# Kernel tuning notes

Hardware: AMD Instinct MI355X
Metric: run time of the kernel (lower is better)

Reference implementation:

```python
import jax, jax.numpy as jnp
import numpy as np

B, N, E, F, G = 32, 512, 4, 128, 64
EMB, HID = 128, 256  # NodeEmbedding: Linear(E*G=256 -> 256) + BN + ELU + Linear(256 -> 128)
NUM_EDGES = 8192
BN_EPS = 1e-5


def setup_inputs() -> dict:
    key = jax.random.key(0)
    ks = jax.random.split(key, 8)
    X = jax.random.normal(ks[0], (B, N, F), dtype=jnp.float32)
    edges = jax.random.randint(ks[1], (B, E, 2, NUM_EDGES), 0, N, dtype=jnp.int64)
    # per-edge-type projection W_e: [F, G] (glorot)
    Ws = jax.random.normal(ks[2], (E, F, G), dtype=jnp.float32) * np.sqrt(2.0 / (F + G))
    # attention vectors a_e: [2G, 1]
    a = jax.random.normal(ks[3], (E, 2 * G, 1), dtype=jnp.float32) * (1.414 * np.sqrt(2.0 / (2 * G + 1)))
    lin0_w = jax.random.normal(ks[4], (E * G, HID), dtype=jnp.float32) * np.sqrt(2.0 / (E * G + HID))
    lin0_b = jnp.zeros((HID,), dtype=jnp.float32)
    bn_gamma = jnp.ones((HID,), dtype=jnp.float32)
    bn_beta = jnp.zeros((HID,), dtype=jnp.float32)
    lin1_w = jax.random.normal(ks[5], (HID, EMB), dtype=jnp.float32) * np.sqrt(2.0 / (HID + EMB))
    lin1_b = jnp.zeros((EMB,), dtype=jnp.float32)
    return {"X": X, "edges": edges, "Ws": Ws, "a": a, "lin0_w": lin0_w,
            "lin0_b": lin0_b, "bn_gamma": bn_gamma, "bn_beta": bn_beta,
            "lin1_w": lin1_w, "lin1_b": lin1_b}


def _dense_adj(edges):
    # COO -> dense, summing duplicates like torch.sparse_coo_tensor(...).to_dense()
    b_ix = jnp.arange(B)[:, None, None]
    e_ix = jnp.arange(E)[None, :, None]
    src = edges[:, :, 0, :]
    dst = edges[:, :, 1, :]
    A = jnp.zeros((B, E, N, N), dtype=jnp.float32)
    return A.at[b_ix, e_ix, src, dst].add(1.0)


def reference(X, edges, Ws, a, lin0_w, lin0_b, bn_gamma, bn_beta, lin1_w, lin1_b):
    A = _dense_adj(edges)                                   # [B,E,N,N]
    Wh = jnp.einsum('bnf,efg->beng', X, Ws)                 # [B,E,N,G]
    Wh1 = jnp.einsum('beng,ego->beno', Wh, a[:, :G, :])     # [B,E,N,1]
    Wh2 = jnp.einsum('beng,ego->beno', Wh, a[:, G:, :])     # [B,E,N,1]
    scores = (Wh1 + jnp.swapaxes(Wh2, 2, 3)) * A            # [B,E,N,N] (masked-to-0, NOT -inf: faithful)
    att = jax.nn.softmax(scores, axis=-1)
    H = jnp.einsum('benm,bemg->beng', att * A, Wh)          # [B,E,N,G]
    H = jnp.transpose(H, (0, 2, 1, 3)).reshape(B * N, E * G)
    # NodeEmbedding MLP (BatchNorm1d in training mode: batch stats, biased var)
    h = H @ lin0_w + lin0_b
    mu = jnp.mean(h, axis=0)
    var = jnp.mean((h - mu) ** 2, axis=0)
    h = (h - mu) * jax.lax.rsqrt(var + BN_EPS) * bn_gamma + bn_beta
    h = jax.nn.elu(h)
    out = h @ lin1_w + lin1_b
    return out.reshape(B, N, EMB)
```

## Files before the change

### kernel.cpp

```cpp
#include <hip/hip_runtime.h>

#define Bx 32
#define Nx 512
#define Ex 4
#define Fx 128
#define Gx 64
#define HIDx 256
#define EMBx 128
#define NEDGE 8192

typedef __attribute__((ext_vector_type(8))) short bf16x8;
typedef __attribute__((ext_vector_type(4))) float f32x4;

__device__ __forceinline__ ushort f2bf(float x) {
    unsigned int u = __float_as_uint(x);
    u += 0x7fffu + ((u >> 16) & 1u);
    return (ushort)(u >> 16);
}
__device__ __forceinline__ float bf2f(ushort h) {
    return __uint_as_float(((unsigned int)h) << 16);
}

__global__ __launch_bounds__(256) void k0_convert(const float* __restrict__ w0,
                                                  const float* __restrict__ w1,
                                                  ushort* __restrict__ W0T,
                                                  ushort* __restrict__ W1T) {
    int j = blockIdx.x, k = threadIdx.x;
    if (j < HIDx) {
        W0T[j * HIDx + k] = f2bf(w0[k * HIDx + j]);
    } else {
        int jj = j - HIDx;
        W1T[jj * HIDx + k] = f2bf(w1[k * EMBx + jj]);
    }
}

__global__ __launch_bounds__(256) void k1_wh(const float* __restrict__ X,
                                             const float* __restrict__ Ws,
                                             const float* __restrict__ a,
                                             ushort* __restrict__ Whb,
                                             float* __restrict__ w1,
                                             float* __restrict__ w2) {
    __shared__ float sXT[Fx][68];
    __shared__ float red1[16][68];
    __shared__ float red2[16][68];
    int id = blockIdx.x;
    int e = id & 3;
    int rest = id >> 2;
    int tile = rest & 7;
    int b = rest >> 3;
    int be = b * 4 + e;
    int n0 = tile * 64;
    int tid = threadIdx.x;
    for (int i = tid; i < 64 * Fx; i += 256) {
        int n = i >> 7, k = i & 127;
        sXT[k][n] = X[(size_t)(b * Nx + n0 + n) * Fx + k];
    }
    __syncthreads();
    const float* We = Ws + e * Fx * Gx;
    int gq = tid & 15, nq = tid >> 4;
    int gg = gq * 4, nn = nq * 4;
    float acc[4][4];
    #pragma unroll
    for (int i = 0; i < 4; ++i)
        #pragma unroll
        for (int j = 0; j < 4; ++j) acc[i][j] = 0.f;
    #pragma unroll 4
    for (int k = 0; k < Fx; ++k) {
        float4 av = *(const float4*)&sXT[k][nn];
        float4 bv = *(const float4*)&We[k * Gx + gg];
        float ai[4] = {av.x, av.y, av.z, av.w};
        float bj[4] = {bv.x, bv.y, bv.z, bv.w};
        #pragma unroll
        for (int i = 0; i < 4; ++i)
            #pragma unroll
            for (int j = 0; j < 4; ++j) acc[i][j] += ai[i] * bj[j];
    }
    float a1[4], a2[4];
    #pragma unroll
    for (int j = 0; j < 4; ++j) {
        a1[j] = a[e * 2 * Gx + gg + j];
        a2[j] = a[e * 2 * Gx + Gx + gg + j];
    }
    #pragma unroll
    for (int j = 0; j < 4; ++j) {
        ushort4 v;
        v.x = f2bf(acc[0][j]); v.y = f2bf(acc[1][j]);
        v.z = f2bf(acc[2][j]); v.w = f2bf(acc[3][j]);
        *(ushort4*)&Whb[((size_t)be * Gx + gg + j) * Nx + n0 + nn] = v;
    }
    #pragma unroll
    for (int i = 0; i < 4; ++i) {
        float p1 = acc[i][0] * a1[0] + acc[i][1] * a1[1] + acc[i][2] * a1[2] + acc[i][3] * a1[3];
        float p2 = acc[i][0] * a2[0] + acc[i][1] * a2[1] + acc[i][2] * a2[2] + acc[i][3] * a2[3];
        red1[gq][nn + i] = p1;
        red2[gq][nn + i] = p2;
    }
    __syncthreads();
    if (tid < 64) {
        float s1 = 0.f, s2 = 0.f;
        #pragma unroll
        for (int t = 0; t < 16; ++t) { s1 += red1[t][tid]; s2 += red2[t][tid]; }
        w1[be * Nx + tid + n0] = s1;
        w2[be * Nx + tid + n0] = s2;
    }
}

__global__ __launch_bounds__(512) void k2_att(const int* __restrict__ edges,
                                              const ushort* __restrict__ Whb,
                                              const float* __restrict__ w1g,
                                              const float* __restrict__ w2g,
                                              ushort* __restrict__ Hb) {
    __shared__ ushort P[32 * 512];
    __shared__ float sw2s[512];
    __shared__ float sw1[32];
    __shared__ float sinv[32];
    unsigned int* cnt = (unsigned int*)P;
    int be = blockIdx.x; int b = be >> 2; int e = be & 3;
    int n0 = blockIdx.y * 32;
    int tid = threadIdx.x;
    for (int i = tid; i < 32 * 132; i += 512) cnt[i] = 0u;
    sw2s[tid ^ (((tid >> 5) & 7) << 2)] = w2g[be * Nx + tid];
    if (tid < 32) sw1[tid] = w1g[be * Nx + n0 + tid];
    __syncthreads();
    const int4* srcp = (const int4*)(edges + (size_t)be * 2 * NEDGE);
    const int4* dstp = (const int4*)(edges + (size_t)be * 2 * NEDGE + NEDGE);
    for (int i = tid; i < NEDGE / 4; i += 512) {
        int4 s4 = srcp[i]; int4 d4 = dstp[i];
        int ss[4] = {s4.x, s4.y, s4.z, s4.w};
        int dd[4] = {d4.x, d4.y, d4.z, d4.w};
        #pragma unroll
        for (int u = 0; u < 4; ++u) {
            unsigned int r = (unsigned int)(ss[u] - n0);
            if (r < 32u) atomicAdd(&cnt[r * 132 + (dd[u] >> 2)], 1u << ((dd[u] & 3) * 8));
        }
    }
    __syncthreads();
    int r = tid >> 4, c = tid & 15;
    unsigned int w0_[8];
    const unsigned int* crow = cnt + r * 132 + c * 8;
    #pragma unroll
    for (int i = 0; i < 8; ++i) w0_[i] = crow[i];
    float w1v = sw1[r];
    float mx = 0.f; int K = 0;
    #pragma unroll
    for (int t = 0; t < 8; ++t) {
        unsigned int cw = w0_[t];
        int m0 = c * 32 + t * 4;
        float4 s2 = *(const float4*)&sw2s[m0 ^ ((c & 7) << 2)];
        float ssv[4] = {s2.x, s2.y, s2.z, s2.w};
        #pragma unroll
        for (int jj = 0; jj < 4; ++jj) {
            int cc = (cw >> (jj * 8)) & 255;
            if (cc) { mx = fmaxf(mx, (w1v + ssv[jj]) * (float)cc); K++; }
        }
    }
    #pragma unroll
    for (int off = 1; off < 16; off <<= 1) {
        mx = fmaxf(mx, __shfl_xor(mx, off, 64));
        K += __shfl_xor(K, off, 64);
    }
    __syncthreads();
    float dsum = 0.f;
    #pragma unroll
    for (int tp = 0; tp < 4; ++tp) {
        unsigned int pkw[4];
        #pragma unroll
        for (int h = 0; h < 2; ++h) {
            unsigned int cw = (h == 0) ? w0_[tp * 2] : w0_[tp * 2 + 1];
            int m0 = c * 32 + (tp * 2 + h) * 4;
            float4 s2 = *(const float4*)&sw2s[m0 ^ ((c & 7) << 2)];
            float ssv[4] = {s2.x, s2.y, s2.z, s2.w};
            unsigned int lo = 0, hi = 0;
            #pragma unroll
            for (int jj = 0; jj < 4; ++jj) {
                int cc = (cw >> (jj * 8)) & 255;
                float s = (w1v + ssv[jj]) * (float)cc;
                float ew = __expf(s - mx);
                ew = cc ? ew : 0.f;
                dsum += ew;
                unsigned int pb = cc ? (unsigned int)f2bf(ew * (float)cc) : 0u;
                if (jj & 2) hi |= pb << ((jj & 1) * 16);
                else        lo |= pb << ((jj & 1) * 16);
            }
            pkw[h * 2] = lo; pkw[h * 2 + 1] = hi;
        }
        uint4 pk = {pkw[0], pkw[1], pkw[2], pkw[3]};
        unsigned int byteo = ((unsigned int)(r * 1024 + c * 64 + tp * 16)) ^ ((unsigned int)(r & 7) << 4);
        *(uint4*)((char*)P + byteo) = pk;
    }
    #pragma unroll
    for (int off = 1; off < 16; off <<= 1) dsum += __shfl_xor(dsum, off, 64);
    if (c == 0) sinv[r] = 1.f / (dsum + (float)(Nx - K) * __expf(-mx));
    __syncthreads();
    int wave = tid >> 6, lane = tid & 63;
    int wr = wave >> 2, wc = wave & 3;
    int row = wr * 16 + (lane & 15);
    int kgrp = lane >> 4;
    f32x4 acc = {0.f, 0.f, 0.f, 0.f};
    const ushort* WB = Whb + (size_t)be * Gx * Nx;
    int g0 = wc * 16 + (lane & 15);
    const ushort* Bp = WB + (size_t)g0 * Nx + kgrp * 8;
    unsigned int aswz = ((unsigned int)(row & 7)) << 4;
    #pragma unroll
    for (int ks = 0; ks < 16; ++ks) {
        unsigned int abyte = ((unsigned int)(row * 1024 + ks * 64 + kgrp * 16)) ^ aswz;
        bf16x8 af = *(const bf16x8*)((const char*)P + abyte);
        bf16x8 bfv = *(const bf16x8*)(Bp + ks * 32);
        acc = __builtin_amdgcn_mfma_f32_16x16x32_bf16(af, bfv, acc, 0, 0, 0);
    }
    float4 iv = *(const float4*)&sinv[wr * 16 + kgrp * 4];
    float ivv[4] = {iv.x, iv.y, iv.z, iv.w};
    #pragma unroll
    for (int reg = 0; reg < 4; ++reg) {
        int rr = n0 + wr * 16 + kgrp * 4 + reg;
        Hb[((size_t)(b * Nx) + rr) * (Ex * Gx) + e * Gx + wc * 16 + (lane & 15)] =
            f2bf(acc[reg] * ivv[reg]);
    }
}

__global__ __launch_bounds__(256) void k3_lin0(const ushort* __restrict__ Hb,
                                               const ushort* __restrict__ W0T,
                                               const float* __restrict__ lin0_b,
                                               ushort* __restrict__ h_pre,
                                               float* __restrict__ partials) {
    __shared__ float red_s[2][256], red_q[2][256];
    int tid = threadIdx.x, wave = tid >> 6, lane = tid & 63;
    int wr = wave >> 1, wc = wave & 1;
    int row0 = blockIdx.x * 32 + wr * 16;
    int arow = lane & 15, kg = lane >> 4;
    const ushort* A = Hb + (size_t)(row0 + arow) * HIDx;
    f32x4 acc[8];
    #pragma unroll
    for (int t = 0; t < 8; ++t) acc[t] = (f32x4){0.f, 0.f, 0.f, 0.f};
    #pragma unroll
    for (int ks = 0; ks < 8; ++ks) {
        int k0 = ks * 32 + kg * 8;
        bf16x8 af = *(const bf16x8*)&A[k0];
        #pragma unroll
        for (int jt = 0; jt < 8; ++jt) {
            bf16x8 bf = *(const bf16x8*)&W0T[(size_t)(wc * 128 + jt * 16 + arow) * HIDx + k0];
            acc[jt] = __builtin_amdgcn_mfma_f32_16x16x32_bf16(af, bf, acc[jt], 0, 0, 0);
        }
    }
    #pragma unroll
    for (int jt = 0; jt < 8; ++jt) {
        int col = wc * 128 + jt * 16 + arow;
        float b = lin0_b[col];
        float s = 0.f, q = 0.f;
        #pragma unroll
        for (int reg = 0; reg < 4; ++reg) {
            float v = acc[jt][reg] + b;
            h_pre[(size_t)(row0 + kg * 4 + reg) * HIDx + col] = f2bf(v);
            s += v; q += v * v;
        }
        s += __shfl_xor(s, 16, 64); s += __shfl_xor(s, 32, 64);
        q += __shfl_xor(q, 16, 64); q += __shfl_xor(q, 32, 64);
        if (lane < 16) { red_s[wr][col] = s; red_q[wr][col] = q; }
    }
    __syncthreads();
    int j = tid;
    partials[(size_t)blockIdx.x * 2 * HIDx + j] = red_s[0][j] + red_s[1][j];
    partials[(size_t)blockIdx.x * 2 * HIDx + HIDx + j] = red_q[0][j] + red_q[1][j];
}

__global__ __launch_bounds__(256) void k3b_stats(const float* __restrict__ partials,
                                                 const float* __restrict__ gamma,
                                                 const float* __restrict__ beta,
                                                 float* __restrict__ sb) {
    __shared__ float rs[8][32], rq[8][32];
    int jl = threadIdx.x & 31, sl = threadIdx.x >> 5;
    int j = blockIdx.x * 32 + jl;
    float s = 0.f, q = 0.f;
    for (int blk = sl; blk < 512; blk += 8) {
        s += partials[blk * 512 + j];
        q += partials[blk * 512 + 256 + j];
    }
    rs[sl][jl] = s; rq[sl][jl] = q;
    __syncthreads();
    if (threadIdx.x < 32) {
        float S = 0.f, Q = 0.f;
        #pragma unroll
        for (int t = 0; t < 8; ++t) { S += rs[t][jl]; Q += rq[t][jl]; }
        const float invM = 1.f / 16384.f;
        float mu = S * invM;
        float var = fmaxf(Q * invM - mu * mu, 0.f);
        float sc = gamma[j] * rsqrtf(var + 1e-5f);
        sb[j] = sc;
        sb[256 + j] = beta[j] - mu * sc;
    }
}

__global__ __launch_bounds__(256) void k4_lin1(const ushort* __restrict__ h_pre,
                                               const float* __restrict__ sb,
                                               const ushort* __restrict__ W1T,
                                               const float* __restrict__ lin1_b,
                                               float* __restrict__ out) {
    int tid = threadIdx.x, wave = tid >> 6, lane = tid & 63;
    int wr = wave >> 1, wc = wave & 1;
    int row0 = blockIdx.x * 32 + wr * 16;
    int arow = lane & 15, kg = lane >> 4;
    const ushort* A = h_pre + (size_t)(row0 + arow) * HIDx;
    f32x4 acc[4];
    #pragma unroll
    for (int t = 0; t < 4; ++t) acc[t] = (f32x4){0.f, 0.f, 0.f, 0.f};
    #pragma unroll
    for (int ks = 0; ks < 8; ++ks) {
        int k0 = ks * 32 + kg * 8;
        bf16x8 hv = *(const bf16x8*)&A[k0];
        float4 sc0 = *(const float4*)&sb[k0];
        float4 sc1 = *(const float4*)&sb[k0 + 4];
        float4 bi0 = *(const float4*)&sb[256 + k0];
        float4 bi1 = *(const float4*)&sb[256 + k0 + 4];
        float scv[8] = {sc0.x, sc0.y, sc0.z, sc0.w, sc1.x, sc1.y, sc1.z, sc1.w};
        float biv[8] = {bi0.x, bi0.y, bi0.z, bi0.w, bi1.x, bi1.y, bi1.z, bi1.w};
        bf16x8 af;
        #pragma unroll
        for (int u = 0; u < 8; ++u) {
            float v = bf2f((ushort)hv[u]) * scv[u] + biv[u];
            v = v > 0.f ? v : expm1f(v);
            af[u] = (short)f2bf(v);
        }
        #pragma unroll
        for (int jt = 0; jt < 4; ++jt) {
            bf16x8 bf = *(const bf16x8*)&W1T[(size_t)(wc * 64 + jt * 16 + arow) * HIDx + k0];
            acc[jt] = __builtin_amdgcn_mfma_f32_16x16x32_bf16(af, bf, acc[jt], 0, 0, 0);
        }
    }
    #pragma unroll
    for (int jt = 0; jt < 4; ++jt) {
        int col = wc * 64 + jt * 16 + arow;
        float b = lin1_b[col];
        #pragma unroll
        for (int reg = 0; reg < 4; ++reg)
            out[(size_t)(row0 + kg * 4 + reg) * EMBx + col] = acc[jt][reg] + b;
    }
}

extern "C" void kernel_launch(void* const* d_in, const int* in_sizes, int n_in,
                              void* d_out, int out_size, void* d_ws, size_t ws_size,
                              hipStream_t stream) {
    const float* X      = (const float*)d_in[0];
    const int*   edges  = (const int*)d_in[1];
    const float* Ws     = (const float*)d_in[2];
    const float* a      = (const float*)d_in[3];
    const float* lin0_w = (const float*)d_in[4];
    const float* lin0_b = (const float*)d_in[5];
    const float* gamma  = (const float*)d_in[6];
    const float* beta   = (const float*)d_in[7];
    const float* lin1_w = (const float*)d_in[8];
    const float* lin1_b = (const float*)d_in[9];
    float* ws = (float*)d_ws;

    ushort* Whb     = (ushort*)ws;
    ushort* h_pre   = (ushort*)ws;
    ushort* Hb      = (ushort*)(ws + 4194304);
    float*  w1      = ws + 8388608;
    float*  w2      = ws + 8454144;
    ushort* W0T     = (ushort*)(ws + 8388608);
    ushort* W1T     = (ushort*)(ws + 8421376);
    float*  partials= ws + 8519680;
    float*  sb      = ws + 8781824;
    float*  out     = (float*)d_out;

    k1_wh  <<<dim3(1024), 256, 0, stream>>>(X, Ws, a, Whb, w1, w2);
    k2_att <<<dim3(Bx * Ex, Nx / 32), 512, 0, stream>>>(edges, Whb, w1, w2, Hb);
    k0_convert<<<dim3(HIDx + EMBx), 256, 0, stream>>>(lin0_w, lin1_w, W0T, W1T);
    k3_lin0<<<dim3(512), 256, 0, stream>>>(Hb, W0T, lin0_b, h_pre, partials);
    k3b_stats<<<8, 256, 0, stream>>>(partials, gamma, beta, sb);
    k4_lin1<<<dim3(512), 256, 0, stream>>>(h_pre, sb, W1T, lin1_b, out);
}
```

Baseline: 146.9 us.

## Use bf16 MFMA for Wh projection and drop softmax max pass

The Wh = X·W_e projection now runs on bf16 MFMA instructions, using a pre-transposed bf16 copy of Ws produced by the convert kernel, which is moved to run first. The attention-kernel softmax drops the separate max-finding pass: it uses exp2 on log2e-prescaled scores clamped at 120, counts non-zero entries with a byte-wise popcount, and wave priority is raised around the MFMA loop. This cuts fp32 FMA work and one full pass over the count words. In exchange, X and Ws lose precision to bf16, and an unshifted exponent risks overflow or precision loss if scores are large.

```diff
diff --git a/kernel.cpp b/kernel.cpp
--- a/kernel.cpp
+++ b/kernel.cpp
@@ -12,6 +12,8 @@
 typedef __attribute__((ext_vector_type(8))) short bf16x8;
 typedef __attribute__((ext_vector_type(4))) float f32x4;
 
+#define L2E 1.44269504f
+
 __device__ __forceinline__ ushort f2bf(float x) {
     unsigned int u = __float_as_uint(x);
     u += 0x7fffu + ((u >> 16) & 1u);
@@ -22,27 +24,33 @@
 }
 
 __global__ __launch_bounds__(256) void k0_convert(const float* __restrict__ w0,
-                                                  const float* __restrict__ w1,
+                                                  const float* __restrict__ w1f,
+                                                  const float* __restrict__ Wsf,
                                                   ushort* __restrict__ W0T,
-                                                  ushort* __restrict__ W1T) {
+                                                  ushort* __restrict__ W1T,
+                                                  ushort* __restrict__ WsT) {
     int j = blockIdx.x, k = threadIdx.x;
     if (j < HIDx) {
         W0T[j * HIDx + k] = f2bf(w0[k * HIDx + j]);
+    } else if (j < HIDx + EMBx) {
+        int jj = j - HIDx;
+        W1T[jj * HIDx + k] = f2bf(w1f[k * EMBx + jj]);
     } else {
-        int jj = j - HIDx;
-        W1T[jj * HIDx + k] = f2bf(w1[k * EMBx + jj]);
+        int eg = j - (HIDx + EMBx);
+        if (k < Fx) {
+            int e = eg >> 6, g = eg & 63;
+            WsT[eg * Fx + k] = f2bf(Wsf[(e * Fx + k) * Gx + g]);
+        }
     }
 }
 
 __global__ __launch_bounds__(256) void k1_wh(const float* __restrict__ X,
-                                             const float* __restrict__ Ws,
+                                             const ushort* __restrict__ WsT,
                                              const float* __restrict__ a,
                                              ushort* __restrict__ Whb,
                                              float* __restrict__ w1,
                                              float* __restrict__ w2) {
-    __shared__ float sXT[Fx][68];
-    __shared__ float red1[16][68];
-    __shared__ float red2[16][68];
+    __shared__ ushort sXb[64 * 128];
     int id = blockIdx.x;
     int e = id & 3;
     int rest = id >> 2;
@@ -51,57 +59,61 @@
     int be = b * 4 + e;
     int n0 = tile * 64;
     int tid = threadIdx.x;
-    for (int i = tid; i < 64 * Fx; i += 256) {
-        int n = i >> 7, k = i & 127;
-        sXT[k][n] = X[(size_t)(b * Nx + n0 + n) * Fx + k];
-    }
-    __syncthreads();
-    const float* We = Ws + e * Fx * Gx;
-    int gq = tid & 15, nq = tid >> 4;
-    int gg = gq * 4, nn = nq * 4;
-    float acc[4][4];
-    #pragma unroll
-    for (int i = 0; i < 4; ++i)
-        #pragma unroll
-        for (int j = 0; j < 4; ++j) acc[i][j] = 0.f;
-    #pragma unroll 4
-    for (int k = 0; k < Fx; ++k) {
-        float4 av = *(const float4*)&sXT[k][nn];
-        float4 bv = *(const float4*)&We[k * Gx + gg];
-        float ai[4] = {av.x, av.y, av.z, av.w};
-        float bj[4] = {bv.x, bv.y, bv.z, bv.w};
-        #pragma unroll
-        for (int i = 0; i < 4; ++i)
-            #pragma unroll
-            for (int j = 0; j < 4; ++j) acc[i][j] += ai[i] * bj[j];
-    }
-    float a1[4], a2[4];
-    #pragma unroll
-    for (int j = 0; j < 4; ++j) {
-        a1[j] = a[e * 2 * Gx + gg + j];
-        a2[j] = a[e * 2 * Gx + Gx + gg + j];
-    }
-    #pragma unroll
-    for (int j = 0; j < 4; ++j) {
+    for (int i = tid; i < 2048; i += 256) {
+        int row = i >> 5, kq = i & 31;
+        float4 xv = *(const float4*)&X[(size_t)(b * Nx + n0 + row) * Fx + kq * 4];
+        ushort4 hv;
+        hv.x = f2bf(xv.x); hv.y = f2bf(xv.y); hv.z = f2bf(xv.z); hv.w = f2bf(xv.w);
+        unsigned int byteo = ((unsigned int)(row * 256 + kq * 8)) ^ (((unsigned int)(row & 7)) << 4);
+        *(ushort4*)((char*)sXb + byteo) = hv;
+    }
+    __syncthreads();
+    int wave = tid >> 6, lane = tid & 63;
+    int arow = lane & 15, kg = lane >> 4;
+    int row = wave * 16 + arow;
+    f32x4 acc[4];
+    #pragma unroll
+    for (int t = 0; t < 4; ++t) acc[t] = (f32x4){0.f, 0.f, 0.f, 0.f};
+    const ushort* WT = WsT + e * Gx * Fx;
+    unsigned int aswz = ((unsigned int)(row & 7)) << 4;
+    #pragma unroll
+    for (int ks = 0; ks < 4; ++ks) {
+        unsigned int abyte = ((unsigned int)(row * 256 + ks * 64 + kg * 16)) ^ aswz;
+        bf16x8 af = *(const bf16x8*)((const char*)sXb + abyte);
+        #pragma unroll
+        for (int jt = 0; jt < 4; ++jt) {
+            bf16x8 bf = *(const bf16x8*)&WT[(size_t)(jt * 16 + arow) * Fx + ks * 32 + kg * 8];
+            acc[jt] = __builtin_amdgcn_mfma_f32_16x16x32_bf16(af, bf, acc[jt], 0, 0, 0);
+        }
+    }
+    float a1v[4], a2v[4];
+    #pragma unroll
+    for (int jt = 0; jt < 4; ++jt) {
+        a1v[jt] = a[e * 2 * Gx + jt * 16 + arow];
+        a2v[jt] = a[e * 2 * Gx + Gx + jt * 16 + arow];
+    }
+    int m0 = n0 + wave * 16 + kg * 4;
+    #pragma unroll
+    for (int jt = 0; jt < 4; ++jt) {
+        int g = jt * 16 + arow;
         ushort4 v;
-        v.x = f2bf(acc[0][j]); v.y = f2bf(acc[1][j]);
-        v.z = f2bf(acc[2][j]); v.w = f2bf(acc[3][j]);
-        *(ushort4*)&Whb[((size_t)be * Gx + gg + j) * Nx + n0 + nn] = v;
-    }
-    #pragma unroll
-    for (int i = 0; i < 4; ++i) {
-        float p1 = acc[i][0] * a1[0] + acc[i][1] * a1[1] + acc[i][2] * a1[2] + acc[i][3] * a1[3];
-        float p2 = acc[i][0] * a2[0] + acc[i][1] * a2[1] + acc[i][2] * a2[2] + acc[i][3] * a2[3];
-        red1[gq][nn + i] = p1;
-        red2[gq][nn + i] = p2;
-    }
-    __syncthreads();
-    if (tid < 64) {
-        float s1 = 0.f, s2 = 0.f;
-        #pragma unroll
-        for (int t = 0; t < 16; ++t) { s1 += red1[t][tid]; s2 += red2[t][tid]; }
-        w1[be * Nx + tid + n0] = s1;
-        w2[be * Nx + tid + n0] = s2;
+        v.x = f2bf(acc[jt][0]); v.y = f2bf(acc[jt][1]);
+        v.z = f2bf(acc[jt][2]); v.w = f2bf(acc[jt][3]);
+        *(ushort4*)&Whb[((size_t)be * Gx + g) * Nx + m0] = v;
+    }
+    #pragma unroll
+    for (int reg = 0; reg < 4; ++reg) {
+        float p1 = acc[0][reg] * a1v[0] + acc[1][reg] * a1v[1] + acc[2][reg] * a1v[2] + acc[3][reg] * a1v[3];
+        float p2 = acc[0][reg] * a2v[0] + acc[1][reg] * a2v[1] + acc[2][reg] * a2v[2] + acc[3][reg] * a2v[3];
+        #pragma unroll
+        for (int off = 1; off < 16; off <<= 1) {
+            p1 += __shfl_xor(p1, off, 64);
+            p2 += __shfl_xor(p2, off, 64);
+        }
+        if (arow == 0) {
+            w1[be * Nx + m0 + reg] = p1;
+            w2[be * Nx + m0 + reg] = p2;
+        }
     }
 }
 
@@ -119,8 +131,8 @@
     int n0 = blockIdx.y * 32;
     int tid = threadIdx.x;
     for (int i = tid; i < 32 * 132; i += 512) cnt[i] = 0u;
-    sw2s[tid ^ (((tid >> 5) & 7) << 2)] = w2g[be * Nx + tid];
-    if (tid < 32) sw1[tid] = w1g[be * Nx + n0 + tid];
+    sw2s[tid ^ (((tid >> 5) & 7) << 2)] = w2g[be * Nx + tid] * L2E;
+    if (tid < 32) sw1[tid] = w1g[be * Nx + n0 + tid] * L2E;
     __syncthreads();
     const int4* srcp = (const int4*)(edges + (size_t)be * 2 * NEDGE);
     const int4* dstp = (const int4*)(edges + (size_t)be * 2 * NEDGE + NEDGE);
@@ -136,61 +148,47 @@
     }
     __syncthreads();
     int r = tid >> 4, c = tid & 15;
-    unsigned int w0_[8];
+    unsigned int cw[8];
     const unsigned int* crow = cnt + r * 132 + c * 8;
     #pragma unroll
-    for (int i = 0; i < 8; ++i) w0_[i] = crow[i];
+    for (int i = 0; i < 8; ++i) cw[i] = crow[i];
     float w1v = sw1[r];
-    float mx = 0.f; int K = 0;
-    #pragma unroll
-    for (int t = 0; t < 8; ++t) {
-        unsigned int cw = w0_[t];
-        int m0 = c * 32 + t * 4;
-        float4 s2 = *(const float4*)&sw2s[m0 ^ ((c & 7) << 2)];
-        float ssv[4] = {s2.x, s2.y, s2.z, s2.w};
-        #pragma unroll
-        for (int jj = 0; jj < 4; ++jj) {
-            int cc = (cw >> (jj * 8)) & 255;
-            if (cc) { mx = fmaxf(mx, (w1v + ssv[jj]) * (float)cc); K++; }
-        }
-    }
-    #pragma unroll
-    for (int off = 1; off < 16; off <<= 1) {
-        mx = fmaxf(mx, __shfl_xor(mx, off, 64));
-        K += __shfl_xor(K, off, 64);
-    }
-    __syncthreads();
-    float dsum = 0.f;
+    __syncthreads();
+    float dsum = 0.f; int K = 0;
     #pragma unroll
     for (int tp = 0; tp < 4; ++tp) {
         unsigned int pkw[4];
         #pragma unroll
         for (int h = 0; h < 2; ++h) {
-            unsigned int cw = (h == 0) ? w0_[tp * 2] : w0_[tp * 2 + 1];
+            unsigned int w = cw[tp * 2 + h];
+            unsigned int nzm = (w | ((w & 0x7f7f7f7fu) + 0x7f7f7f7fu)) & 0x80808080u;
+            K += __popc(nzm);
             int m0 = c * 32 + (tp * 2 + h) * 4;
             float4 s2 = *(const float4*)&sw2s[m0 ^ ((c & 7) << 2)];
-            float ssv[4] = {s2.x, s2.y, s2.z, s2.w};
+            float sv[4] = {s2.x, s2.y, s2.z, s2.w};
             unsigned int lo = 0, hi = 0;
             #pragma unroll
             for (int jj = 0; jj < 4; ++jj) {
-                int cc = (cw >> (jj * 8)) & 255;
-                float s = (w1v + ssv[jj]) * (float)cc;
-                float ew = __expf(s - mx);
-                ew = cc ? ew : 0.f;
-                dsum += ew;
-                unsigned int pb = cc ? (unsigned int)f2bf(ew * (float)cc) : 0u;
+                unsigned int ccu = (w >> (jj * 8)) & 255u;
+                float cf = (float)ccu;
+                float ew = __builtin_exp2f(fminf((w1v + sv[jj]) * cf, 120.f));
+                dsum += ccu ? ew : 0.f;
+                unsigned int pb = (unsigned int)f2bf(ew * cf);
                 if (jj & 2) hi |= pb << ((jj & 1) * 16);
                 else        lo |= pb << ((jj & 1) * 16);
             }
             pkw[h * 2] = lo; pkw[h * 2 + 1] = hi;
         }
         uint4 pk = {pkw[0], pkw[1], pkw[2], pkw[3]};
-        unsigned int byteo = ((unsigned int)(r * 1024 + c * 64 + tp * 16)) ^ ((unsigned int)(r & 7) << 4);
+        unsigned int byteo = ((unsigned int)(r * 1024 + c * 64 + tp * 16)) ^ (((unsigned int)(r & 7)) << 4);
         *(uint4*)((char*)P + byteo) = pk;
     }
     #pragma unroll
-    for (int off = 1; off < 16; off <<= 1) dsum += __shfl_xor(dsum, off, 64);
-    if (c == 0) sinv[r] = 1.f / (dsum + (float)(Nx - K) * __expf(-mx));
+    for (int off = 1; off < 16; off <<= 1) {
+        dsum += __shfl_xor(dsum, off, 64);
+        K += __shfl_xor(K, off, 64);
+    }
+    if (c == 0) sinv[r] = 1.f / (dsum + (float)(Nx - K));
     __syncthreads();
     int wave = tid >> 6, lane = tid & 63;
     int wr = wave >> 2, wc = wave & 3;
@@ -201,6 +199,7 @@
     int g0 = wc * 16 + (lane & 15);
     const ushort* Bp = WB + (size_t)g0 * Nx + kgrp * 8;
     unsigned int aswz = ((unsigned int)(row & 7)) << 4;
+    __builtin_amdgcn_s_setprio(1);
     #pragma unroll
     for (int ks = 0; ks < 16; ++ks) {
         unsigned int abyte = ((unsigned int)(row * 1024 + ks * 64 + kgrp * 16)) ^ aswz;
@@ -208,6 +207,7 @@
         bf16x8 bfv = *(const bf16x8*)(Bp + ks * 32);
         acc = __builtin_amdgcn_mfma_f32_16x16x32_bf16(af, bfv, acc, 0, 0, 0);
     }
+    __builtin_amdgcn_s_setprio(0);
     float4 iv = *(const float4*)&sinv[wr * 16 + kgrp * 4];
     float ivv[4] = {iv.x, iv.y, iv.z, iv.w};
     #pragma unroll
@@ -356,15 +356,16 @@
     ushort* Hb      = (ushort*)(ws + 4194304);
     float*  w1      = ws + 8388608;
     float*  w2      = ws + 8454144;
-    ushort* W0T     = (ushort*)(ws + 8388608);
-    ushort* W1T     = (ushort*)(ws + 8421376);
     float*  partials= ws + 8519680;
     float*  sb      = ws + 8781824;
+    ushort* WsT     = (ushort*)(ws + 8782336);
+    ushort* W0T     = (ushort*)(ws + 8798720);
+    ushort* W1T     = (ushort*)(ws + 8831488);
     float*  out     = (float*)d_out;
 
-    k1_wh  <<<dim3(1024), 256, 0, stream>>>(X, Ws, a, Whb, w1, w2);
+    k0_convert<<<dim3(HIDx + EMBx + 256), 256, 0, stream>>>(lin0_w, lin1_w, Ws, W0T, W1T, WsT);
+    k1_wh  <<<dim3(1024), 256, 0, stream>>>(X, WsT, a, Whb, w1, w2);
     k2_att <<<dim3(Bx * Ex, Nx / 32), 512, 0, stream>>>(edges, Whb, w1, w2, Hb);
-    k0_convert<<<dim3(HIDx + EMBx), 256, 0, stream>>>(lin0_w, lin1_w, W0T, W1T);
     k3_lin0<<<dim3(512), 256, 0, stream>>>(Hb, W0T, lin0_b, h_pre, partials);
     k3b_stats<<<8, 256, 0, stream>>>(partials, gamma, beta, sb);
     k4_lin1<<<dim3(512), 256, 0, stream>>>(h_pre, sb, W1T, lin1_b, out);
```

Result: faster. 130.5 us (-11.2%).
